# Performance work log

Hardware: AMD Instinct MI355X
Metric: run time of the kernel (lower is better)

Reference implementation:

```python
import jax, jax.numpy as jnp
import numpy as np

# FP8 E4M3 constants (per FP8Handler)
E4M3_MAX = 240.0          # max_normal
MANTISSA_SCALE = 8.0      # 2 ** mantissa_bits (3)
SCALE_EPS = 1e-10


def setup_inputs() -> dict:
    key = jax.random.key(0)
    k1, k2, k3 = jax.random.split(key, 3)
    B, S, D_IN, D_OUT = 4, 2048, 4096, 4096
    x = jax.random.normal(k1, (B, S, D_IN), dtype=jnp.float32)
    weight = jax.random.normal(k2, (D_OUT, D_IN), dtype=jnp.float32)
    bias = jax.random.normal(k3, (D_OUT,), dtype=jnp.float32)
    return {"x": x, "weight": weight, "bias": bias}


def _fp8_e4m3_quant_dequant(w, scale):
    # FP8Handler.quantize_tensor + _simulate_e4m3_precision
    s = jnp.clip(w / scale, -E4M3_MAX, E4M3_MAX)
    s = s.astype(jnp.float16).astype(jnp.float32)  # fp16 round-trip
    q = jnp.round(s * MANTISSA_SCALE) / MANTISSA_SCALE  # mantissa truncation
    q = jnp.clip(q, -E4M3_MAX, E4M3_MAX)
    return q * scale


def reference(x, weight, bias):
    # FP8Quantizer.compute_scale: per-tensor max-abs, margin=0, fresh history
    amax = jnp.max(jnp.abs(weight))
    scale = jnp.maximum(amax / E4M3_MAX, SCALE_EPS)
    qw = _fp8_e4m3_quant_dequant(weight, scale)  # [out, in]
    # F.linear(x, qw, bias): x [b, s, in] @ qw.T [in, out] + bias
    return jnp.einsum('bsi,oi->bso', x, qw) + bias
```

## Files before the change

kernel.cpp:

```cpp
#include <hip/hip_runtime.h>
#include <hip/hip_bf16.h>
#include <hip/hip_fp16.h>

#define E4M3_MAX 240.0f

typedef __attribute__((ext_vector_type(8))) __bf16 bf16x8;
typedef __attribute__((ext_vector_type(4))) float f32x4;
typedef unsigned short ushort_t;

__device__ __forceinline__ void gload_lds16(const void* g, void* l) {
  __builtin_amdgcn_global_load_lds(
      (const __attribute__((address_space(1))) void*)g,
      (__attribute__((address_space(3))) void*)l,
      16, 0, 0);
}

__global__ void amax_abs_kernel(const float* __restrict__ w, int n4,
                                unsigned* __restrict__ amax_bits) {
  float m = 0.0f;
  const float4* w4 = (const float4*)w;
  int stride = gridDim.x * blockDim.x;
  for (int i = blockIdx.x * blockDim.x + threadIdx.x; i < n4; i += stride) {
    float4 v = w4[i];
    m = fmaxf(m, fmaxf(fmaxf(fabsf(v.x), fabsf(v.y)),
                       fmaxf(fabsf(v.z), fabsf(v.w))));
  }
  for (int off = 32; off > 0; off >>= 1)
    m = fmaxf(m, __shfl_down(m, off, 64));
  __shared__ float smax[4];
  int l = threadIdx.x & 63, wv = threadIdx.x >> 6;
  if (l == 0) smax[wv] = m;
  __syncthreads();
  if (threadIdx.x == 0) {
    float bm = fmaxf(fmaxf(smax[0], smax[1]), fmaxf(smax[2], smax[3]));
    atomicMax(amax_bits, __float_as_uint(bm));
  }
}

__global__ void quant_weight_kernel(const float* __restrict__ w,
                                    const unsigned* __restrict__ amax_bits,
                                    ushort_t* __restrict__ qw, int n4) {
  float amax = __uint_as_float(*amax_bits);
  float scale = fmaxf(amax / E4M3_MAX, 1e-10f);
  const float4* w4 = (const float4*)w;
  ushort4* q4 = (ushort4*)qw;
  int stride = gridDim.x * blockDim.x;
  for (int i = blockIdx.x * blockDim.x + threadIdx.x; i < n4; i += stride) {
    float4 v = w4[i];
    float r[4] = {v.x, v.y, v.z, v.w};
    ushort_t o[4];
#pragma unroll
    for (int j = 0; j < 4; ++j) {
      float s = fminf(fmaxf(r[j] / scale, -E4M3_MAX), E4M3_MAX);
      s = __half2float(__float2half(s));
      float q = rintf(s * 8.0f) * 0.125f;
      q = fminf(fmaxf(q, -E4M3_MAX), E4M3_MAX);
      __hip_bfloat16 h = __float2bfloat16(q * scale);
      o[j] = *(ushort_t*)&h;
    }
    ushort4 ov = {o[0], o[1], o[2], o[3]};
    q4[i] = ov;
  }
}

__global__ void cvt_bf16_kernel(const float* __restrict__ x,
                                ushort_t* __restrict__ xb, int n4) {
  const float4* x4 = (const float4*)x;
  ushort4* o4 = (ushort4*)xb;
  int stride = gridDim.x * blockDim.x;
  for (int i = blockIdx.x * blockDim.x + threadIdx.x; i < n4; i += stride) {
    float4 v = x4[i];
    __hip_bfloat16 h0 = __float2bfloat16(v.x);
    __hip_bfloat16 h1 = __float2bfloat16(v.y);
    __hip_bfloat16 h2 = __float2bfloat16(v.z);
    __hip_bfloat16 h3 = __float2bfloat16(v.w);
    ushort4 o = {*(ushort_t*)&h0, *(ushort_t*)&h1,
                 *(ushort_t*)&h2, *(ushort_t*)&h3};
    o4[i] = o;
  }
}


#define BAR() do { asm volatile("" ::: "memory"); \
                   __builtin_amdgcn_s_barrier(); \
                   asm volatile("" ::: "memory"); } while (0)
#define LGKM0() asm volatile("s_waitcnt lgkmcnt(0)" ::: "memory")
#define LGKM8() asm volatile("s_waitcnt lgkmcnt(8)" ::: "memory")
#define VMC(N)  asm volatile("s_waitcnt vmcnt(" #N ")" ::: "memory")

__global__ __launch_bounds__(512, 2) void gemm256_8ph(
    const ushort_t* __restrict__ A, const ushort_t* __restrict__ Bt,
    const float* __restrict__ bias, float* __restrict__ C) {
  constexpr int K = 4096, N = 4096;
  __shared__ __align__(16) ushort_t As[2][2][8192];
  __shared__ __align__(16) ushort_t Bs[2][2][8192];

  const int tid = threadIdx.x;
  const int wid = tid >> 6, lane = tid & 63;
  const int wm = wid >> 2, wn = wid & 3;
  const int lk = lane >> 4, lr = lane & 15;

  int bid = blockIdx.x;
  int swz = (bid & 7) * 64 + (bid >> 3);
  int bm = swz >> 4, bn = swz & 15;

  const ushort_t* Ab = A + (size_t)bm * 256 * K;
  const ushort_t* Bb = Bt + (size_t)bn * 256 * K;

  int offG[2];
#pragma unroll
  for (int q = 0; q < 2; ++q) {
    int s = q * 512 + tid;
    int row = s >> 3;
    int c = (s & 7) ^ (row & 7);
    offG[q] = row * K + c * 8;
  }

#define STAGE_A(buf, half, kt)                                            \
  do { _Pragma("unroll") for (int q = 0; q < 2; ++q)                      \
    gload_lds16(Ab + (size_t)(half) * 128 * K + (kt) * 64 + offG[q],      \
                &As[buf][half][(q * 512 + wid * 64) * 8]); } while (0)
#define STAGE_B(buf, half, kt)                                            \
  do { _Pragma("unroll") for (int q = 0; q < 2; ++q)                      \
    gload_lds16(Bb + (size_t)(half) * 128 * K + (kt) * 64 + offG[q],      \
                &Bs[buf][half][(q * 512 + wid * 64) * 8]); } while (0)

  const int abase = lr * 64;
  const int bbase = (wn & 1) * 4096 + lr * 64;
  const int bhalf = wn >> 1;
  const int xk0 = ((lk) ^ (lr & 7)) * 8;
  const int xk1 = ((4 + lk) ^ (lr & 7)) * 8;

  bf16x8 afr[8][2], bfr[4][2];
  f32x4 acc[8][4] = {};

#define RD_B(buf)                                                         \
  do { _Pragma("unroll") for (int fj = 0; fj < 4; ++fj) {                 \
    bfr[fj][0] = *(const bf16x8*)&Bs[buf][bhalf][bbase + fj * 1024 + xk0];\
    bfr[fj][1] = *(const bf16x8*)&Bs[buf][bhalf][bbase + fj * 1024 + xk1];\
  } } while (0)
#define RD_A(buf, F0, F1)                                                 \
  do { _Pragma("unroll") for (int fi = F0; fi < F1; ++fi) {               \
    afr[fi][0] = *(const bf16x8*)&As[buf][wm][abase + fi * 1024 + xk0];   \
    afr[fi][1] = *(const bf16x8*)&As[buf][wm][abase + fi * 1024 + xk1];   \
  } } while (0)
#define MMA_Q(q)                                                          \
  do { __builtin_amdgcn_s_setprio(1);                                     \
    _Pragma("unroll") for (int fi = (q)*2; fi < (q)*2 + 2; ++fi)          \
      _Pragma("unroll") for (int fj = 0; fj < 4; ++fj) {                  \
        acc[fi][fj] = __builtin_amdgcn_mfma_f32_16x16x32_bf16(            \
            afr[fi][0], bfr[fj][0], acc[fi][fj], 0, 0, 0);                \
        acc[fi][fj] = __builtin_amdgcn_mfma_f32_16x16x32_bf16(            \
            afr[fi][1], bfr[fj][1], acc[fi][fj], 0, 0, 0);                \
      }                                                                   \
    __builtin_amdgcn_s_setprio(0); } while (0)

  STAGE_A(0, 0, 0); STAGE_A(0, 1, 0);
  STAGE_B(0, 0, 0); STAGE_B(0, 1, 0);
  STAGE_A(1, 0, 1); STAGE_A(1, 1, 1);
  VMC(4);
  BAR();

  for (int t = 0; t < 62; t += 2) {
    RD_B(0); RD_A(0, 0, 2);
    STAGE_B(1, 0, t + 1);
    LGKM8(); BAR(); LGKM0(); MMA_Q(0); BAR();
    RD_A(0, 2, 8);
    STAGE_B(1, 1, t + 1);
    LGKM8(); BAR(); LGKM0(); MMA_Q(1); BAR();
    STAGE_A(0, 0, t + 2);
    BAR(); MMA_Q(2); BAR();
    STAGE_A(0, 1, t + 2);
    BAR(); MMA_Q(3); VMC(4); BAR();
    RD_B(1); RD_A(1, 0, 2);
    STAGE_B(0, 0, t + 2);
    LGKM8(); BAR(); LGKM0(); MMA_Q(0); BAR();
    RD_A(1, 2, 8);
    STAGE_B(0, 1, t + 2);
    LGKM8(); BAR(); LGKM0(); MMA_Q(1); BAR();
    STAGE_A(1, 0, t + 3);
    BAR(); MMA_Q(2); BAR();
    STAGE_A(1, 1, t + 3);
    BAR(); MMA_Q(3); VMC(4); BAR();
  }

  RD_B(0); RD_A(0, 0, 2);
  STAGE_B(1, 0, 63);
  LGKM8(); BAR(); LGKM0(); MMA_Q(0); BAR();
  RD_A(0, 2, 8);
  STAGE_B(1, 1, 63);
  LGKM8(); BAR(); LGKM0(); MMA_Q(1); BAR();
  MMA_Q(2); MMA_Q(3);
  VMC(0);
  BAR();
  RD_B(1); RD_A(1, 0, 8);
  LGKM0();
  MMA_Q(0); MMA_Q(1); MMA_Q(2); MMA_Q(3);

  float* Cb = C + (size_t)(bm * 256 + wm * 128) * N + bn * 256 + wn * 64;
#pragma unroll
  for (int fj = 0; fj < 4; ++fj) {
    int n = fj * 16 + lr;
    float bv = bias[bn * 256 + wn * 64 + n];
#pragma unroll
    for (int fi = 0; fi < 8; ++fi) {
      int m0 = fi * 16 + lk * 4;
#pragma unroll
      for (int r = 0; r < 4; ++r)
        Cb[(size_t)(m0 + r) * N + n] = acc[fi][fj][r] + bv;
    }
  }
}

extern "C" void kernel_launch(void* const* d_in, const int* in_sizes, int n_in,
                              void* d_out, int out_size, void* d_ws, size_t ws_size,
                              hipStream_t stream) {
  const float* x = (const float*)d_in[0];
  const float* wt = (const float*)d_in[1];
  const float* bias = (const float*)d_in[2];
  float* out = (float*)d_out;

  const int DIN = 4096;
  const int NW = in_sizes[1];
  const int M = in_sizes[0] / DIN;

  char* ws = (char*)d_ws;
  unsigned* amax_bits = (unsigned*)ws;
  ushort_t* qw = (ushort_t*)(ws + 256);
  ushort_t* xb = (ushort_t*)(ws + 256 + (size_t)NW * 2);

  hipMemsetAsync(amax_bits, 0, 4, stream);
  hipLaunchKernelGGL(amax_abs_kernel, dim3(1024), dim3(256), 0, stream,
                     wt, NW / 4, amax_bits);
  hipLaunchKernelGGL(quant_weight_kernel, dim3(2048), dim3(256), 0, stream,
                     wt, amax_bits, qw, NW / 4);
  hipLaunchKernelGGL(cvt_bf16_kernel, dim3(2048), dim3(256), 0, stream,
                     x, xb, (M * DIN) / 4);

  hipLaunchKernelGGL(gemm256_8ph, dim3(512), dim3(512), 0, stream,
                     xb, qw, bias, out);
}
```

Baseline: 329.4 us.

## Restructure GEMM main loop into register double-buffered k-half pipeline

Rewrites the bf16 GEMM inner loop so that LDS fragment reads for the next k-half or next tile are issued while MFMAs on the current fragments run. A and B fragments are split into ping-pong register sets. Staging is rescheduled to load whole A/B tiles with sched_barriers and finer lgkmcnt waits. The aim is to hide LDS read latency behind MFMA work and to cut barrier-stall phases. In exchange it raises register pressure, and the ordering of the reworked waits and buffer reuse is fragile.

```diff
diff --git a/kernel.cpp b/kernel.cpp
--- a/kernel.cpp
+++ b/kernel.cpp
@@ -84,11 +84,12 @@
 #define BAR() do { asm volatile("" ::: "memory"); \
                    __builtin_amdgcn_s_barrier(); \
                    asm volatile("" ::: "memory"); } while (0)
-#define LGKM0() asm volatile("s_waitcnt lgkmcnt(0)" ::: "memory")
-#define LGKM8() asm volatile("s_waitcnt lgkmcnt(8)" ::: "memory")
-#define VMC(N)  asm volatile("s_waitcnt vmcnt(" #N ")" ::: "memory")
-
-__global__ __launch_bounds__(512, 2) void gemm256_8ph(
+#define LGKM(n) do { asm volatile("s_waitcnt lgkmcnt(" #n ")" ::: "memory"); \
+                     __builtin_amdgcn_sched_barrier(0); } while (0)
+#define VMC(n)  do { asm volatile("s_waitcnt vmcnt(" #n ")" ::: "memory"); \
+                     __builtin_amdgcn_sched_barrier(0); } while (0)
+
+__global__ __launch_bounds__(512, 2) void gemm256_pipe(
     const ushort_t* __restrict__ A, const ushort_t* __restrict__ Bt,
     const float* __restrict__ bias, float* __restrict__ C) {
   constexpr int K = 4096, N = 4096;
@@ -116,14 +117,16 @@
     offG[q] = row * K + c * 8;
   }
 
-#define STAGE_A(buf, half, kt)                                            \
-  do { _Pragma("unroll") for (int q = 0; q < 2; ++q)                      \
-    gload_lds16(Ab + (size_t)(half) * 128 * K + (kt) * 64 + offG[q],      \
-                &As[buf][half][(q * 512 + wid * 64) * 8]); } while (0)
-#define STAGE_B(buf, half, kt)                                            \
-  do { _Pragma("unroll") for (int q = 0; q < 2; ++q)                      \
-    gload_lds16(Bb + (size_t)(half) * 128 * K + (kt) * 64 + offG[q],      \
-                &Bs[buf][half][(q * 512 + wid * 64) * 8]); } while (0)
+#define STAGE_A2(buf, kt)                                                  \
+  do { _Pragma("unroll") for (int h = 0; h < 2; ++h)                       \
+    _Pragma("unroll") for (int q = 0; q < 2; ++q)                          \
+      gload_lds16(Ab + (size_t)h * 128 * K + (kt) * 64 + offG[q],          \
+                  &As[buf][h][(q * 512 + wid * 64) * 8]); } while (0)
+#define STAGE_B2(buf, kt)                                                  \
+  do { _Pragma("unroll") for (int h = 0; h < 2; ++h)                       \
+    _Pragma("unroll") for (int q = 0; q < 2; ++q)                          \
+      gload_lds16(Bb + (size_t)h * 128 * K + (kt) * 64 + offG[q],          \
+                  &Bs[buf][h][(q * 512 + wid * 64) * 8]); } while (0)
 
   const int abase = lr * 64;
   const int bbase = (wn & 1) * 4096 + lr * 64;
@@ -131,71 +134,55 @@
   const int xk0 = ((lk) ^ (lr & 7)) * 8;
   const int xk1 = ((4 + lk) ^ (lr & 7)) * 8;
 
-  bf16x8 afr[8][2], bfr[4][2];
+  bf16x8 afX[4], afY[4], bfE[4], bfO[4];
   f32x4 acc[8][4] = {};
 
-#define RD_B(buf)                                                         \
-  do { _Pragma("unroll") for (int fj = 0; fj < 4; ++fj) {                 \
-    bfr[fj][0] = *(const bf16x8*)&Bs[buf][bhalf][bbase + fj * 1024 + xk0];\
-    bfr[fj][1] = *(const bf16x8*)&Bs[buf][bhalf][bbase + fj * 1024 + xk1];\
-  } } while (0)
-#define RD_A(buf, F0, F1)                                                 \
-  do { _Pragma("unroll") for (int fi = F0; fi < F1; ++fi) {               \
-    afr[fi][0] = *(const bf16x8*)&As[buf][wm][abase + fi * 1024 + xk0];   \
-    afr[fi][1] = *(const bf16x8*)&As[buf][wm][abase + fi * 1024 + xk1];   \
-  } } while (0)
-#define MMA_Q(q)                                                          \
-  do { __builtin_amdgcn_s_setprio(1);                                     \
-    _Pragma("unroll") for (int fi = (q)*2; fi < (q)*2 + 2; ++fi)          \
-      _Pragma("unroll") for (int fj = 0; fj < 4; ++fj) {                  \
-        acc[fi][fj] = __builtin_amdgcn_mfma_f32_16x16x32_bf16(            \
-            afr[fi][0], bfr[fj][0], acc[fi][fj], 0, 0, 0);                \
-        acc[fi][fj] = __builtin_amdgcn_mfma_f32_16x16x32_bf16(            \
-            afr[fi][1], bfr[fj][1], acc[fi][fj], 0, 0, 0);                \
-      }                                                                   \
-    __builtin_amdgcn_s_setprio(0); } while (0)
-
-  STAGE_A(0, 0, 0); STAGE_A(0, 1, 0);
-  STAGE_B(0, 0, 0); STAGE_B(0, 1, 0);
-  STAGE_A(1, 0, 1); STAGE_A(1, 1, 1);
+#define RD_A(dst, buf, fi0, xkv)                                           \
+  do { _Pragma("unroll") for (int i = 0; i < 4; ++i)                       \
+    dst[i] = *(const bf16x8*)&As[buf][wm][abase + ((fi0) + i) * 1024 + (xkv)]; } while (0)
+#define RD_B4(dst, buf, xkv)                                               \
+  do { _Pragma("unroll") for (int j = 0; j < 4; ++j)                       \
+    dst[j] = *(const bf16x8*)&Bs[buf][bhalf][bbase + j * 1024 + (xkv)]; } while (0)
+#define RD_B2(dst, j0, buf, xkv)                                           \
+  do { _Pragma("unroll") for (int j = 0; j < 2; ++j)                       \
+    dst[(j0) + j] = *(const bf16x8*)&Bs[buf][bhalf][bbase + ((j0) + j) * 1024 + (xkv)]; } while (0)
+
+#define MMA(areg, breg, H)                                                 \
+  do { __builtin_amdgcn_s_setprio(1);                                      \
+    _Pragma("unroll") for (int i = 0; i < 4; ++i)                          \
+      _Pragma("unroll") for (int j = 0; j < 4; ++j)                        \
+        acc[(H) * 4 + i][j] = __builtin_amdgcn_mfma_f32_16x16x32_bf16(     \
+            areg[i], breg[j], acc[(H) * 4 + i][j], 0, 0, 0);               \
+    __builtin_amdgcn_s_setprio(0);                                         \
+    __builtin_amdgcn_sched_barrier(0); } while (0)
+
+#define TILE(buf, obuf, t, DO_SA, DO_SB, LAST)                             \
+  do {                                                                     \
+    RD_A(afY, buf, 4, xk0); RD_B2(bfO, 0, buf, xk1);                       \
+    if (DO_SA) STAGE_A2(obuf, (t) + 1);                                    \
+    LGKM(6); MMA(afX, bfE, 0); BAR();                                      \
+    RD_A(afX, buf, 0, xk1); RD_B2(bfO, 2, buf, xk1);                       \
+    LGKM(6); MMA(afY, bfE, 1); BAR();                                      \
+    RD_A(afY, buf, 4, xk1);                                                \
+    LGKM(4); MMA(afX, bfO, 0); VMC(0); BAR();                              \
+    if (!(LAST)) { RD_A(afX, obuf, 0, xk0); RD_B4(bfE, obuf, xk0); }       \
+    if (DO_SB) STAGE_B2(buf, (t) + 2);                                     \
+    if (!(LAST)) { LGKM(8); MMA(afY, bfO, 1); BAR(); }                     \
+    else         { LGKM(0); MMA(afY, bfO, 1); }                            \
+  } while (0)
+
+  STAGE_A2(0, 0); STAGE_B2(0, 0);
+  STAGE_B2(1, 1);
   VMC(4);
   BAR();
+  RD_A(afX, 0, 0, xk0); RD_B4(bfE, 0, xk0);
 
   for (int t = 0; t < 62; t += 2) {
-    RD_B(0); RD_A(0, 0, 2);
-    STAGE_B(1, 0, t + 1);
-    LGKM8(); BAR(); LGKM0(); MMA_Q(0); BAR();
-    RD_A(0, 2, 8);
-    STAGE_B(1, 1, t + 1);
-    LGKM8(); BAR(); LGKM0(); MMA_Q(1); BAR();
-    STAGE_A(0, 0, t + 2);
-    BAR(); MMA_Q(2); BAR();
-    STAGE_A(0, 1, t + 2);
-    BAR(); MMA_Q(3); VMC(4); BAR();
-    RD_B(1); RD_A(1, 0, 2);
-    STAGE_B(0, 0, t + 2);
-    LGKM8(); BAR(); LGKM0(); MMA_Q(0); BAR();
-    RD_A(1, 2, 8);
-    STAGE_B(0, 1, t + 2);
-    LGKM8(); BAR(); LGKM0(); MMA_Q(1); BAR();
-    STAGE_A(1, 0, t + 3);
-    BAR(); MMA_Q(2); BAR();
-    STAGE_A(1, 1, t + 3);
-    BAR(); MMA_Q(3); VMC(4); BAR();
-  }
-
-  RD_B(0); RD_A(0, 0, 2);
-  STAGE_B(1, 0, 63);
-  LGKM8(); BAR(); LGKM0(); MMA_Q(0); BAR();
-  RD_A(0, 2, 8);
-  STAGE_B(1, 1, 63);
-  LGKM8(); BAR(); LGKM0(); MMA_Q(1); BAR();
-  MMA_Q(2); MMA_Q(3);
-  VMC(0);
-  BAR();
-  RD_B(1); RD_A(1, 0, 8);
-  LGKM0();
-  MMA_Q(0); MMA_Q(1); MMA_Q(2); MMA_Q(3);
+    TILE(0, 1, t, 1, 1, 0);
+    TILE(1, 0, t + 1, 1, 1, 0);
+  }
+  TILE(0, 1, 62, 1, 0, 0);
+  TILE(1, 0, 63, 0, 0, 1);
 
   float* Cb = C + (size_t)(bm * 256 + wm * 128) * N + bn * 256 + wn * 64;
 #pragma unroll
@@ -237,6 +224,6 @@
   hipLaunchKernelGGL(cvt_bf16_kernel, dim3(2048), dim3(256), 0, stream,
                      x, xb, (M * DIN) / 4);
 
-  hipLaunchKernelGGL(gemm256_8ph, dim3(512), dim3(512), 0, stream,
+  hipLaunchKernelGGL(gemm256_pipe, dim3(512), dim3(512), 0, stream,
                      xb, qw, bias, out);
 }
```

Measured after the change: 364.9 us. +10.8%, slower.
